# Performance work log

Hardware: AMD Instinct MI355X
Metric: run time of the kernel (lower is better)

## Reference

```python
import jax, jax.numpy as jnp
import numpy as np

N_NODES = 50000
N_EDGES = 1600000
HEADS = 4
EMB = 16          # per-head output features
HIDDEN = 256
BATCH = 1024
IN_FEAT = 4       # num_node_features (hard-coded in source)
NEG_SLOPE = 0.2   # PyG GATConv default leaky_relu slope


def setup_inputs() -> dict:
    key = jax.random.key(0)
    ks = jax.random.split(key, 8)
    out_dim = HEADS * EMB
    return {
        "message": jax.random.normal(ks[0], (BATCH, HIDDEN), dtype=jnp.float32),
        "x": jax.random.normal(ks[1], (N_NODES, IN_FEAT), dtype=jnp.float32),
        "edge_index": jax.random.randint(ks[2], (2, N_EDGES), 0, N_NODES, dtype=jnp.int64)
                      if jax.config.read("jax_enable_x64") else
                      jax.random.randint(ks[2], (2, N_EDGES), 0, N_NODES, dtype=jnp.int32),
        "gat_w": jax.random.normal(ks[3], (IN_FEAT, out_dim), dtype=jnp.float32) * 0.5,
        "att_src": jax.random.normal(ks[4], (HEADS, EMB), dtype=jnp.float32) * 0.25,
        "att_dst": jax.random.normal(ks[5], (HEADS, EMB), dtype=jnp.float32) * 0.25,
        "gat_b": jnp.zeros((out_dim,), dtype=jnp.float32),
        "fc_w": jax.random.normal(ks[6], (HIDDEN, out_dim), dtype=jnp.float32) * (1.0 / np.sqrt(HIDDEN)),
        "fc_b": jnp.zeros((out_dim,), dtype=jnp.float32),
    }


def reference(message, x, edge_index, gat_w, att_src, att_dst, gat_b, fc_w, fc_b):
    N = x.shape[0]
    H, F = att_src.shape
    src, dst = edge_index[0], edge_index[1]

    # --- GATConv (single layer, concat heads) ---
    h = (x @ gat_w).reshape(N, H, F)                       # [N,H,F]
    a_s = jnp.einsum('nhf,hf->nh', h, att_src)             # per-node src score
    a_d = jnp.einsum('nhf,hf->nh', h, att_dst)             # per-node dst score
    e = jax.nn.leaky_relu(a_s[src] + a_d[dst], NEG_SLOPE)  # [E,H]

    # stable softmax over edges grouped by destination node
    m = jax.ops.segment_max(e, dst, num_segments=N)        # [N,H]
    ex = jnp.exp(e - m[dst])                               # [E,H]
    denom = jax.ops.segment_sum(ex, dst, num_segments=N)   # [N,H]
    alpha = ex / (denom[dst] + 1e-16)                      # [E,H]

    # weighted aggregation of source features into destinations
    agg = jax.ops.segment_sum(alpha[:, :, None] * h[src], dst, num_segments=N)  # [N,H,F]
    h_out = agg.reshape(N, H * F) + gat_b                  # [N, H*F]

    # --- fc + matmul + log_softmax ---
    msg_emb = message @ fc_w + fc_b                        # [B, H*F]
    logits = (h_out @ msg_emb.T).T                         # [B, N]
    return jax.nn.log_softmax(logits, axis=1)
```

## Files before the change

### kernel.cpp

```cpp
#include <hip/hip_runtime.h>
#include <math.h>

#define N_NODES 50000
#define N_EDGES 1600000
#define HEADS 4
#define EMB 16
#define HOUT 64
#define HIDDEN 256
#define BATCH 1024
#define NEG_SLOPE 0.2f
#define ATS 50176
#define CHK 512
#define NCH 98
#define SCAN_NB 196
#define NXCD 8
#define DRANGE 6250

__device__ __forceinline__ float lrelu(float x) { return x > 0.f ? x : NEG_SLOPE * x; }

__global__ void k_msgemb(const float* __restrict__ msg, const float* __restrict__ fcw,
                         const float* __restrict__ fcb, const float* __restrict__ gatb,
                         float* __restrict__ msg_emb, float* __restrict__ msgT,
                         float* __restrict__ cvec) {
    __shared__ float mrow[HIDDEN];
    int b = blockIdx.x;
    int j = threadIdx.x;
    for (int k = j; k < HIDDEN; k += 64) mrow[k] = msg[b * HIDDEN + k];
    __syncthreads();
    float acc = fcb[j];
    #pragma unroll 8
    for (int k = 0; k < HIDDEN; k++) acc += mrow[k] * fcw[k * HOUT + j];
    msg_emb[b * HOUT + j] = acc;
    msgT[j * BATCH + b] = acc;
    float cv = gatb[j] * acc;
    for (int o = 32; o > 0; o >>= 1) cv += __shfl_down(cv, o);
    if (j == 0) cvec[b] = cv;
}

__global__ void k_node(const float* __restrict__ x, const float* __restrict__ gatw,
                       const float* __restrict__ atts, const float* __restrict__ attd,
                       float* __restrict__ h, float* __restrict__ a_s, float* __restrict__ a_d) {
    int tid = blockIdx.x * blockDim.x + threadIdx.x;
    int n = tid >> 6;
    int j = tid & 63;
    if (n >= N_NODES) return;
    float4 xv = ((const float4*)x)[n];
    float hv = xv.x * gatw[j] + xv.y * gatw[64 + j] + xv.z * gatw[128 + j] + xv.w * gatw[192 + j];
    h[n * 64 + j] = hv;
    float s = hv * atts[j];
    float d = hv * attd[j];
    for (int o = 8; o > 0; o >>= 1) {
        s += __shfl_down(s, o, 16);
        d += __shfl_down(d, o, 16);
    }
    if ((j & 15) == 0) {
        int head = j >> 4;
        a_s[n * 4 + head] = s;
        a_d[n * 4 + head] = d;
    }
}

__global__ void k_count(const int* __restrict__ ei, int* __restrict__ cnt) {
    int e = blockIdx.x * blockDim.x + threadIdx.x;
    if (e < N_EDGES) atomicAdd(&cnt[ei[N_EDGES + e]], 1);
}

__global__ void k_scan1(const int* __restrict__ cnt, int* __restrict__ localx,
                        int* __restrict__ partial) {
    int b = blockIdx.x, t = threadIdx.x;
    int i = b * 256 + t;
    int v = (i < N_NODES) ? cnt[i] : 0;
    int lane = t & 63, w = t >> 6;
    int sv = v;
    #pragma unroll
    for (int o = 1; o < 64; o <<= 1) {
        int u = __shfl_up(sv, o);
        if (lane >= o) sv += u;
    }
    __shared__ int wsums[4];
    if (lane == 63) wsums[w] = sv;
    __syncthreads();
    int woff = 0;
    #pragma unroll
    for (int k = 0; k < 4; k++) woff += (k < w) ? wsums[k] : 0;
    if (i < N_NODES) localx[i] = woff + sv - v;
    if (t == 0) partial[b] = wsums[0] + wsums[1] + wsums[2] + wsums[3];
}

__global__ void k_scan2(const int* __restrict__ partial, int* __restrict__ blockoff,
                        int* __restrict__ rowptr_last) {
    int t = threadIdx.x;
    int v = (t < SCAN_NB) ? partial[t] : 0;
    int lane = t & 63, w = t >> 6;
    int sv = v;
    #pragma unroll
    for (int o = 1; o < 64; o <<= 1) {
        int u = __shfl_up(sv, o);
        if (lane >= o) sv += u;
    }
    __shared__ int wsums[4];
    if (lane == 63) wsums[w] = sv;
    __syncthreads();
    int woff = 0;
    #pragma unroll
    for (int k = 0; k < 4; k++) woff += (k < w) ? wsums[k] : 0;
    int excl = woff + sv - v;
    if (t < SCAN_NB) blockoff[t] = excl;
    if (t == 255) rowptr_last[0] = excl + v;
}

__global__ void k_scan3(const int* __restrict__ localx, const int* __restrict__ blockoff,
                        int* __restrict__ rowptr, int* __restrict__ cursor) {
    int i = blockIdx.x * 256 + threadIdx.x;
    if (i < N_NODES) {
        int r = localx[i] + blockoff[blockIdx.x];
        rowptr[i] = r;
        cursor[i] = r;
    }
}

__global__ void k_scatter(const int* __restrict__ ei, int* __restrict__ cursor, int* __restrict__ csr) {
    int p = blockIdx.x & 7;
    int tile = blockIdx.x >> 3;
    int e = tile * 256 + threadIdx.x;
    if (e < N_EDGES) {
        int d = ei[N_EDGES + e];
        if ((unsigned)(d - p * DRANGE) < (unsigned)DRANGE) {
            int pos = atomicAdd(&cursor[d], 1);
            csr[pos] = ei[e];
        }
    }
}

__global__ __launch_bounds__(256, 8) void k_agg(const int* __restrict__ rowptr,
                      const int* __restrict__ csr,
                      const float* __restrict__ a_s, const float* __restrict__ a_d,
                      const float* __restrict__ h, float* __restrict__ agg) {
    __shared__ float salpha[4][64];
    int wid = threadIdx.x >> 6;
    int lane = threadIdx.x & 63;
    int n = blockIdx.x * 4 + wid;
    if (n >= N_NODES) return;
    int beg = rowptr[n], end = rowptr[n + 1];
    int head = lane & 3, eoff = lane >> 2;
    float adh = a_d[n * 4 + head];

    float s = 0.f;
    for (int i = beg + eoff; i < end; i += 16) {
        int src = csr[i];
        s += __expf(lrelu(a_s[src * 4 + head] + adh));
    }
    #pragma unroll
    for (int o = 4; o < 64; o <<= 1) s += __shfl_xor(s, o);
    float inv = 1.f / (s + 1e-16f);

    float acc = 0.f;
    const float* ap = &salpha[wid][(lane >> 4) * 16];
    for (int base = beg; base < end; base += 16) {
        int e = base + eoff;
        int ec = (e < end) ? e : (end - 1);
        int src = csr[ec];
        float ev = lrelu(a_s[src * 4 + head] + adh);
        float alpha = (e < end) ? __expf(ev) * inv : 0.f;
        salpha[wid][head * 16 + eoff] = alpha;
        __builtin_amdgcn_wave_barrier();
        #pragma unroll
        for (int c = 0; c < 4; c++) {
            float4 av = *(const float4*)(ap + c * 4);
            int s0 = __builtin_amdgcn_readlane(src, c * 16 + 0);
            int s1 = __builtin_amdgcn_readlane(src, c * 16 + 4);
            int s2 = __builtin_amdgcn_readlane(src, c * 16 + 8);
            int s3 = __builtin_amdgcn_readlane(src, c * 16 + 12);
            acc = fmaf(av.x, h[(size_t)s0 * 64 + lane], acc);
            acc = fmaf(av.y, h[(size_t)s1 * 64 + lane], acc);
            acc = fmaf(av.z, h[(size_t)s2 * 64 + lane], acc);
            acc = fmaf(av.w, h[(size_t)s3 * 64 + lane], acc);
        }
        __builtin_amdgcn_wave_barrier();
    }
    agg[(size_t)n * 64 + lane] = acc;
}

__global__ void k_transpose(const float* __restrict__ agg, float* __restrict__ aggT) {
    __shared__ float tile[64][65];
    int t = threadIdx.x;
    int n0 = blockIdx.x * 64;
    #pragma unroll
    for (int i = 0; i < 16; i++) {
        int idx = i * 256 + t;
        int nl = idx >> 6, f = idx & 63;
        int n = n0 + nl;
        tile[nl][f] = (n < N_NODES) ? agg[(size_t)n * 64 + f] : 0.f;
    }
    __syncthreads();
    int c = n0 >> 9;
    int nb = n0 & 511;
    #pragma unroll
    for (int i = 0; i < 16; i++) {
        int idx = i * 256 + t;
        int f = idx >> 6, nl = idx & 63;
        aggT[(size_t)c * (64 * CHK) + f * CHK + nb + nl] = tile[nl][f];
    }
}

__global__ __launch_bounds__(256, 6) void k_logits(const float* __restrict__ aggT,
    const float* __restrict__ msgT, const float* __restrict__ cvec,
    float* __restrict__ out, float* __restrict__ ps) {
    __shared__ float red_s[16][4];
    int t = threadIdx.x;
    int bg = blockIdx.x;
    int chunk = blockIdx.y;
    const float* ap = aggT + (size_t)chunk * (64 * CHK) + 2 * t;
    const float* mp = msgT + bg * 16;

    float acc0[16], acc1[16];
    #pragma unroll
    for (int b = 0; b < 16; b++) { acc0[b] = 0.f; acc1[b] = 0.f; }

    #pragma unroll 4
    for (int k = 0; k < 64; k++) {
        float2 av = *(const float2*)(ap + (size_t)k * CHK);
        const float* mrow = mp + k * BATCH;
        #pragma unroll
        for (int b = 0; b < 16; b++) {
            float m = mrow[b];
            acc0[b] = fmaf(av.x, m, acc0[b]);
            acc1[b] = fmaf(av.y, m, acc1[b]);
        }
    }

    int n = chunk * CHK + 2 * t;
    bool valid = (n < N_NODES);
    int lane = t & 63, w = t >> 6;
    #pragma unroll
    for (int b = 0; b < 16; b++) {
        int bglob = bg * 16 + b;
        float sc = cvec[bglob];
        float ls = 0.f;
        if (valid) {
            float l0 = acc0[b] + sc;
            float l1 = acc1[b] + sc;
            *(float2*)(out + (size_t)bglob * N_NODES + n) = make_float2(l0, l1);
            ls = __expf(l0) + __expf(l1);
        }
        #pragma unroll
        for (int o = 1; o < 64; o <<= 1) ls += __shfl_xor(ls, o);
        if (lane == 0) red_s[b][w] = ls;
    }
    __syncthreads();
    if (t < 16) {
        float S = red_s[t][0] + red_s[t][1] + red_s[t][2] + red_s[t][3];
        ps[(bg * 16 + t) * NCH + chunk] = S;
    }
}

__global__ void k_rowstats(const float* __restrict__ ps, float* __restrict__ rowls) {
    int b = blockIdx.x * blockDim.x + threadIdx.x;
    if (b >= BATCH) return;
    float S = 0.f;
    for (int i = 0; i < NCH; i++) S += ps[b * NCH + i];
    rowls[b] = logf(S);
}

__global__ void k_fix(float* __restrict__ out, const float* __restrict__ rowls) {
    int idx = blockIdx.x * blockDim.x + threadIdx.x;
    int b = idx / 12500;
    float sub = rowls[b];
    float4 v = ((float4*)out)[idx];
    v.x -= sub; v.y -= sub; v.z -= sub; v.w -= sub;
    ((float4*)out)[idx] = v;
}

extern "C" void kernel_launch(void* const* d_in, const int* in_sizes, int n_in,
                              void* d_out, int out_size, void* d_ws, size_t ws_size,
                              hipStream_t stream) {
    const float* message = (const float*)d_in[0];
    const float* x       = (const float*)d_in[1];
    const int*   ei      = (const int*)d_in[2];
    const float* gat_w   = (const float*)d_in[3];
    const float* att_src = (const float*)d_in[4];
    const float* att_dst = (const float*)d_in[5];
    const float* gat_b   = (const float*)d_in[6];
    const float* fc_w    = (const float*)d_in[7];
    const float* fc_b    = (const float*)d_in[8];
    float* out = (float*)d_out;

    float* ws      = (float*)d_ws;
    float* msg_emb = ws;
    float* msgT    = msg_emb + BATCH * HOUT;
    float* cvec    = msgT + HOUT * BATCH;
    float* a_s     = cvec + BATCH;
    float* a_d     = a_s + (size_t)N_NODES * HEADS;
    float* agg     = a_d + (size_t)N_NODES * HEADS;
    float* hbuf    = agg + (size_t)N_NODES * HOUT;
    float* aggT    = hbuf;
    float* ps      = hbuf + (size_t)HOUT * ATS;
    float* rowls   = ps + BATCH * NCH;
    int*   cnt     = (int*)(rowls + BATCH);
    int*   rowptr  = cnt + N_NODES;
    int*   cursor  = rowptr + N_NODES + 1;
    int*   csr     = cursor + N_NODES;
    int*   localx  = csr + N_EDGES;
    int*   partial = localx + N_NODES;
    int*   blockoff= partial + SCAN_NB;

    hipMemsetAsync(cnt, 0, N_NODES * sizeof(int), stream);
    k_msgemb<<<BATCH, 64, 0, stream>>>(message, fc_w, fc_b, gat_b, msg_emb, msgT, cvec);
    k_node<<<(N_NODES * 64 + 255) / 256, 256, 0, stream>>>(x, gat_w, att_src, att_dst, hbuf, a_s, a_d);
    k_count<<<N_EDGES / 256, 256, 0, stream>>>(ei, cnt);
    k_scan1<<<SCAN_NB, 256, 0, stream>>>(cnt, localx, partial);
    k_scan2<<<1, 256, 0, stream>>>(partial, blockoff, rowptr + N_NODES);
    k_scan3<<<SCAN_NB, 256, 0, stream>>>(localx, blockoff, rowptr, cursor);
    k_scatter<<<NXCD * (N_EDGES / 256), 256, 0, stream>>>(ei, cursor, csr);
    k_agg<<<(N_NODES + 3) / 4, 256, 0, stream>>>(rowptr, csr, a_s, a_d, hbuf, agg);
    k_transpose<<<ATS / 64, 256, 0, stream>>>(agg, aggT);
    dim3 g4(64, NCH);
    k_logits<<<g4, 256, 0, stream>>>(aggT, msgT, cvec, out, ps);
    k_rowstats<<<4, 256, 0, stream>>>(ps, rowls);
    k_fix<<<(BATCH * N_NODES / 4 + 255) / 256, 256, 0, stream>>>(out, rowls);
}
```

Baseline: 577.9 us.

## Recompute logits in second pass to avoid output read-modify-write; partition count atomics by XCD

```diff
diff --git a/kernel.cpp b/kernel.cpp
--- a/kernel.cpp
+++ b/kernel.cpp
@@ -61,8 +61,14 @@
 }
 
 __global__ void k_count(const int* __restrict__ ei, int* __restrict__ cnt) {
-    int e = blockIdx.x * blockDim.x + threadIdx.x;
-    if (e < N_EDGES) atomicAdd(&cnt[ei[N_EDGES + e]], 1);
+    int p = blockIdx.x & 7;
+    int tile = blockIdx.x >> 3;
+    int e = tile * 256 + threadIdx.x;
+    if (e < N_EDGES) {
+        int d = ei[N_EDGES + e];
+        if ((unsigned)(d - p * DRANGE) < (unsigned)DRANGE)
+            atomicAdd(&cnt[d], 1);
+    }
 }
 
 __global__ void k_scan1(const int* __restrict__ cnt, int* __restrict__ localx,
@@ -203,9 +209,9 @@
     }
 }
 
-__global__ __launch_bounds__(256, 6) void k_logits(const float* __restrict__ aggT,
+__global__ __launch_bounds__(256, 6) void k_logsum(const float* __restrict__ aggT,
     const float* __restrict__ msgT, const float* __restrict__ cvec,
-    float* __restrict__ out, float* __restrict__ ps) {
+    float* __restrict__ ps) {
     __shared__ float red_s[16][4];
     int t = threadIdx.x;
     int bg = blockIdx.x;
@@ -237,12 +243,7 @@
         int bglob = bg * 16 + b;
         float sc = cvec[bglob];
         float ls = 0.f;
-        if (valid) {
-            float l0 = acc0[b] + sc;
-            float l1 = acc1[b] + sc;
-            *(float2*)(out + (size_t)bglob * N_NODES + n) = make_float2(l0, l1);
-            ls = __expf(l0) + __expf(l1);
-        }
+        if (valid) ls = __expf(acc0[b] + sc) + __expf(acc1[b] + sc);
         #pragma unroll
         for (int o = 1; o < 64; o <<= 1) ls += __shfl_xor(ls, o);
         if (lane == 0) red_s[b][w] = ls;
@@ -262,13 +263,40 @@
     rowls[b] = logf(S);
 }
 
-__global__ void k_fix(float* __restrict__ out, const float* __restrict__ rowls) {
-    int idx = blockIdx.x * blockDim.x + threadIdx.x;
-    int b = idx / 12500;
-    float sub = rowls[b];
-    float4 v = ((float4*)out)[idx];
-    v.x -= sub; v.y -= sub; v.z -= sub; v.w -= sub;
-    ((float4*)out)[idx] = v;
+__global__ __launch_bounds__(256, 6) void k_logits_w(const float* __restrict__ aggT,
+    const float* __restrict__ msgT, const float* __restrict__ cvec,
+    const float* __restrict__ rowls, float* __restrict__ out) {
+    int t = threadIdx.x;
+    int bg = blockIdx.x;
+    int chunk = blockIdx.y;
+    const float* ap = aggT + (size_t)chunk * (64 * CHK) + 2 * t;
+    const float* mp = msgT + bg * 16;
+
+    float acc0[16], acc1[16];
+    #pragma unroll
+    for (int b = 0; b < 16; b++) { acc0[b] = 0.f; acc1[b] = 0.f; }
+
+    #pragma unroll 4
+    for (int k = 0; k < 64; k++) {
+        float2 av = *(const float2*)(ap + (size_t)k * CHK);
+        const float* mrow = mp + k * BATCH;
+        #pragma unroll
+        for (int b = 0; b < 16; b++) {
+            float m = mrow[b];
+            acc0[b] = fmaf(av.x, m, acc0[b]);
+            acc1[b] = fmaf(av.y, m, acc1[b]);
+        }
+    }
+
+    int n = chunk * CHK + 2 * t;
+    if (n >= N_NODES) return;
+    #pragma unroll
+    for (int b = 0; b < 16; b++) {
+        int bglob = bg * 16 + b;
+        float sub = cvec[bglob] - rowls[bglob];
+        *(float2*)(out + (size_t)bglob * N_NODES + n) =
+            make_float2(acc0[b] + sub, acc1[b] + sub);
+    }
 }
 
 extern "C" void kernel_launch(void* const* d_in, const int* in_sizes, int n_in,
@@ -307,7 +335,7 @@
     hipMemsetAsync(cnt, 0, N_NODES * sizeof(int), stream);
     k_msgemb<<<BATCH, 64, 0, stream>>>(message, fc_w, fc_b, gat_b, msg_emb, msgT, cvec);
     k_node<<<(N_NODES * 64 + 255) / 256, 256, 0, stream>>>(x, gat_w, att_src, att_dst, hbuf, a_s, a_d);
-    k_count<<<N_EDGES / 256, 256, 0, stream>>>(ei, cnt);
+    k_count<<<NXCD * (N_EDGES / 256), 256, 0, stream>>>(ei, cnt);
     k_scan1<<<SCAN_NB, 256, 0, stream>>>(cnt, localx, partial);
     k_scan2<<<1, 256, 0, stream>>>(partial, blockoff, rowptr + N_NODES);
     k_scan3<<<SCAN_NB, 256, 0, stream>>>(localx, blockoff, rowptr, cursor);
@@ -315,7 +343,7 @@
     k_agg<<<(N_NODES + 3) / 4, 256, 0, stream>>>(rowptr, csr, a_s, a_d, hbuf, agg);
     k_transpose<<<ATS / 64, 256, 0, stream>>>(agg, aggT);
     dim3 g4(64, NCH);
-    k_logits<<<g4, 256, 0, stream>>>(aggT, msgT, cvec, out, ps);
+    k_logsum<<<g4, 256, 0, stream>>>(aggT, msgT, cvec, ps);
     k_rowstats<<<4, 256, 0, stream>>>(ps, rowls);
-    k_fix<<<(BATCH * N_NODES / 4 + 255) / 256, 256, 0, stream>>>(out, rowls);
-}
+    k_logits_w<<<g4, 256, 0, stream>>>(aggT, msgT, cvec, rowls, out);
+}
```

Measured after the change: 602.5 us. +4.3%, slower.
